# Optimization experiments

Measured on AMD Instinct MI355X. Metric: run time of the kernel, lower is better.

The kernel has to match this reference:

```python
import jax, jax.numpy as jnp
import numpy as np

IN_F = 4096
OUT_F = 4096
RANK = 16
N_BITS = 4
ALPHA = 1.0
GROUP = 128
Q_N = -(2 ** (N_BITS - 1))       # -8 for 4-bit signed
Q_P = 2 ** (N_BITS - 1) - 1      # +7
EPS = 1e-9


def setup_inputs() -> dict:
    key = jax.random.key(0)
    k0, k1, k2, k3, k4, k5 = jax.random.split(key, 6)
    x = jax.random.normal(k0, (8, 1024, IN_F), dtype=jnp.float32)
    w0 = jax.random.normal(k1, (OUT_F, IN_F), dtype=jnp.float32) * 0.02
    lora_a = jax.random.normal(k2, (RANK, IN_F), dtype=jnp.float32) * 0.02
    lora_b = jax.random.normal(k3, (OUT_F, RANK), dtype=jnp.float32) * 0.02
    num_groups = (OUT_F * IN_F) // GROUP
    q_scale = jnp.abs(jax.random.normal(k4, (num_groups,), dtype=jnp.float32)) * 0.01 + 0.005
    bias = jax.random.normal(k5, (OUT_F,), dtype=jnp.float32) * 0.01
    return {"x": x, "w0": w0, "lora_a": lora_a, "lora_b": lora_b,
            "q_scale": q_scale, "bias": bias}


def _quantize_weight(w0, lora_a, lora_b, q_scale):
    # LoRA merge: w_comb = w0 + alpha * (B @ A)   -> (OUT_F, IN_F)
    w_comb = w0 + ALPHA * (lora_b @ lora_a)
    num_groups = w_comb.size // GROUP
    w_g = w_comb.reshape(num_groups, GROUP)          # grouped view
    s = q_scale[:, None]                             # (G, 1) per-group scale
    w_scaled = w_g / (s + EPS)
    clamped = jnp.clip(w_scaled, Q_N, Q_P)
    q_int = jnp.round(clamped)
    w_q = (q_int * s).reshape(w_comb.shape)          # dequantized fake-quant weight
    return w_q


def reference(x, w0, lora_a, lora_b, q_scale, bias):
    w_q = _quantize_weight(w0, lora_a, lora_b, q_scale)
    # F.linear(x, w_q) + bias : (B, S, IN) @ (IN, OUT)
    return jnp.einsum('bsi,oi->bso', x, w_q) + bias
```

## Files before the change

### kernel.cpp

```cpp
#include <hip/hip_runtime.h>
#include <hip/hip_bf16.h>
#include <stdint.h>
#include <stddef.h>

#define IN_F   4096
#define OUT_F  4096
#define RANK   16
#define GROUP  128
#define M_TOT  8192

#define BM     256
#define BN     256
#define BK     32
#define NIT    (IN_F / BK)
#define HALF_B 16384
#define TILE_B 32768
#define LDS_B  (3 * TILE_B)

typedef __bf16 bf16_t;
typedef __bf16 bf16x4 __attribute__((ext_vector_type(4)));
typedef __bf16 bf16x8 __attribute__((ext_vector_type(8)));
typedef float  f32x4  __attribute__((ext_vector_type(4)));

__device__ static inline void load_lds16(const void* g, void* l) {
  __builtin_amdgcn_global_load_lds(
      (const __attribute__((address_space(1))) unsigned int*)g,
      (__attribute__((address_space(3))) unsigned int*)l,
      16, 0, 0);
}

__global__ void __launch_bounds__(256)
quant_kernel(const float* __restrict__ w0, const float* __restrict__ la,
             const float* __restrict__ lb, const float* __restrict__ qs,
             bf16_t* __restrict__ wq)
{
  const int o = blockIdx.y;
  const int i = blockIdx.x * 1024 + threadIdx.x * 4;

  __shared__ float lbr[RANK];
  if (threadIdx.x < RANK) lbr[threadIdx.x] = lb[o * RANK + threadIdx.x];
  __syncthreads();

  const size_t off = (size_t)o * IN_F + i;
  const float4 w = *(const float4*)(w0 + off);
  float a0 = w.x, a1 = w.y, a2 = w.z, a3 = w.w;
  #pragma unroll
  for (int r = 0; r < RANK; ++r) {
    const float4 av = *(const float4*)(la + (size_t)r * IN_F + i);
    const float bv = lbr[r];
    a0 = fmaf(bv, av.x, a0);
    a1 = fmaf(bv, av.y, a1);
    a2 = fmaf(bv, av.z, a2);
    a3 = fmaf(bv, av.w, a3);
  }
  const float s   = qs[o * (IN_F / GROUP) + (i >> 7)];
  const float inv = 1.0f / (s + 1e-9f);
  const float q0 = rintf(fminf(fmaxf(a0 * inv, -8.0f), 7.0f)) * s;
  const float q1 = rintf(fminf(fmaxf(a1 * inv, -8.0f), 7.0f)) * s;
  const float q2 = rintf(fminf(fmaxf(a2 * inv, -8.0f), 7.0f)) * s;
  const float q3 = rintf(fminf(fmaxf(a3 * inv, -8.0f), 7.0f)) * s;
  bf16x4 v;
  v[0] = (bf16_t)q0; v[1] = (bf16_t)q1; v[2] = (bf16_t)q2; v[3] = (bf16_t)q3;
  *(bf16x4*)(wq + off) = v;
}

__global__ void __launch_bounds__(256)
castx_kernel(const float* __restrict__ x, bf16_t* __restrict__ xb)
{
  const size_t i = ((size_t)blockIdx.x * 256 + threadIdx.x) * 8;
  const float4 a = *(const float4*)(x + i);
  const float4 b = *(const float4*)(x + i + 4);
  bf16x8 v;
  v[0] = (bf16_t)a.x; v[1] = (bf16_t)a.y; v[2] = (bf16_t)a.z; v[3] = (bf16_t)a.w;
  v[4] = (bf16_t)b.x; v[5] = (bf16_t)b.y; v[6] = (bf16_t)b.z; v[7] = (bf16_t)b.w;
  *(bf16x8*)(xb + i) = v;
}

__global__ void __launch_bounds__(512, 2)
gemm_kernel(const bf16_t* __restrict__ A, const bf16_t* __restrict__ Bw,
            const float* __restrict__ bias, float* __restrict__ C)
{
  extern __shared__ __align__(16) char smem[];

  const int tid  = threadIdx.x;
  const int lane = tid & 63;
  const int lr   = lane & 15;
  const int quad = lane >> 4;
  const int wid  = tid >> 6;
  const int wm   = wid >> 2;
  const int wn   = wid & 3;

  const int bid = blockIdx.x;
  const int swz = (bid & 7) * 64 + (bid >> 3);
  const int m0  = (swz >> 4) * BM;
  const int n0  = (swz & 15) * BN;

  const int srow = tid >> 2;
  const int scol = ((tid & 3) ^ ((tid >> 3) & 3)) * 8;
  const bf16_t* gA0 = A  + (size_t)(m0 + srow) * IN_F + scol;
  const bf16_t* gA1 = gA0 + (size_t)128 * IN_F;
  const bf16_t* gB0 = Bw + (size_t)(n0 + srow) * IN_F + scol;
  const bf16_t* gB1 = gB0 + (size_t)128 * IN_F;

  const int rswz = (quad ^ ((lr >> 1) & 3)) * 16;
  const int aOff = (wm * 128 + lr) * 64 + rswz;
  const int bOff = (wn * 64  + lr) * 64 + rswz;

  f32x4 acc[8][4];
  #pragma unroll
  for (int i = 0; i < 8; ++i)
    #pragma unroll
    for (int j = 0; j < 4; ++j)
      acc[i][j] = (f32x4){0.f, 0.f, 0.f, 0.f};

  {
    char* b0 = smem;
    char* b1 = smem + TILE_B;
    load_lds16(gA0,      b0 + tid * 16);
    load_lds16(gA1,      b0 + tid * 16 + 8192);
    load_lds16(gB0,      b0 + HALF_B + tid * 16);
    load_lds16(gB1,      b0 + HALF_B + tid * 16 + 8192);
    load_lds16(gA0 + BK, b1 + tid * 16);
    load_lds16(gA1 + BK, b1 + tid * 16 + 8192);
    load_lds16(gB0 + BK, b1 + HALF_B + tid * 16);
    load_lds16(gB1 + BK, b1 + HALF_B + tid * 16 + 8192);
    asm volatile("s_waitcnt vmcnt(4)" ::: "memory");
    __builtin_amdgcn_s_barrier();
  }

  int rb = 0, wb = 2;
  for (int t = 0; t < NIT; ++t) {
    const char* rA   = smem + rb * TILE_B;
    const char* rB   = rA + HALF_B;
    char*       wbuf = smem + wb * TILE_B;

    bf16x8 bfr[4];
    #pragma unroll
    for (int fn = 0; fn < 4; ++fn)
      bfr[fn] = *(const bf16x8*)(rB + bOff + fn * 1024);
    bf16x8 af[4];
    #pragma unroll
    for (int f = 0; f < 4; ++f)
      af[f] = *(const bf16x8*)(rA + aOff + f * 1024);

    if (t + 2 < NIT) {
      const size_t ko = (size_t)(t + 2) * BK;
      load_lds16(gA0 + ko, wbuf + tid * 16);
      load_lds16(gA1 + ko, wbuf + tid * 16 + 8192);
    }

    __builtin_amdgcn_s_barrier();
    asm volatile("s_waitcnt lgkmcnt(0)" ::: "memory");
    __builtin_amdgcn_sched_barrier(0);
    __builtin_amdgcn_s_setprio(1);
    #pragma unroll
    for (int fm = 0; fm < 4; ++fm)
      #pragma unroll
      for (int fn = 0; fn < 4; ++fn)
        acc[fm][fn] = __builtin_amdgcn_mfma_f32_16x16x32_bf16(
            af[fm], bfr[fn], acc[fm][fn], 0, 0, 0);
    __builtin_amdgcn_s_setprio(0);
    __builtin_amdgcn_s_barrier();

    #pragma unroll
    for (int f = 0; f < 4; ++f)
      af[f] = *(const bf16x8*)(rA + aOff + 4096 + f * 1024);

    if (t + 2 < NIT) {
      const size_t ko = (size_t)(t + 2) * BK;
      load_lds16(gB0 + ko, wbuf + HALF_B + tid * 16);
      load_lds16(gB1 + ko, wbuf + HALF_B + tid * 16 + 8192);
    }

    if (t + 2 < NIT) asm volatile("s_waitcnt vmcnt(4)" ::: "memory");
    else             asm volatile("s_waitcnt vmcnt(0)" ::: "memory");
    __builtin_amdgcn_s_barrier();
    asm volatile("s_waitcnt lgkmcnt(0)" ::: "memory");
    __builtin_amdgcn_sched_barrier(0);
    __builtin_amdgcn_s_setprio(1);
    #pragma unroll
    for (int fm = 0; fm < 4; ++fm)
      #pragma unroll
      for (int fn = 0; fn < 4; ++fn)
        acc[4 + fm][fn] = __builtin_amdgcn_mfma_f32_16x16x32_bf16(
            af[fm], bfr[fn], acc[4 + fm][fn], 0, 0, 0);
    __builtin_amdgcn_s_setprio(0);
    __builtin_amdgcn_s_barrier();

    rb = rb + 1; if (rb == 3) rb = 0;
    wb = wb + 1; if (wb == 3) wb = 0;
  }

  #pragma unroll
  for (int fn = 0; fn < 4; ++fn) {
    const int gn = n0 + wn * 64 + fn * 16 + lr;
    const float bv = bias[gn];
    #pragma unroll
    for (int fm = 0; fm < 8; ++fm) {
      const int gm = m0 + wm * 128 + fm * 16 + quad * 4;
      #pragma unroll
      for (int r = 0; r < 4; ++r)
        C[(size_t)(gm + r) * OUT_F + gn] = acc[fm][fn][r] + bv;
    }
  }
}

extern "C" void kernel_launch(void* const* d_in, const int* in_sizes, int n_in,
                              void* d_out, int out_size, void* d_ws, size_t ws_size,
                              hipStream_t stream) {
  const float* x    = (const float*)d_in[0];
  const float* w0   = (const float*)d_in[1];
  const float* la   = (const float*)d_in[2];
  const float* lb   = (const float*)d_in[3];
  const float* qs   = (const float*)d_in[4];
  const float* bias = (const float*)d_in[5];
  float* out = (float*)d_out;

  bf16_t* wq = (bf16_t*)d_ws;
  bf16_t* xb = (bf16_t*)((char*)d_ws + (size_t)OUT_F * IN_F * 2);

  static bool attr_done = false;
  if (!attr_done) {
    (void)hipFuncSetAttribute((const void*)gemm_kernel,
                              hipFuncAttributeMaxDynamicSharedMemorySize,
                              LDS_B);
    attr_done = true;
  }

  quant_kernel<<<dim3(IN_F / 1024, OUT_F), 256, 0, stream>>>(w0, la, lb, qs, wq);
  castx_kernel<<<(M_TOT * IN_F) / (256 * 8), 256, 0, stream>>>(x, xb);
  gemm_kernel<<<dim3((M_TOT / BM) * (OUT_F / BN)), 512, LDS_B, stream>>>(
      xb, wq, bias, out);
}
```

Measured before the change: 549.6 us.

## Software-pipeline LDS fragment reads ahead of MFMA with register double buffering

Restructures the GEMM main loop so the LDS reads for the next half-tile and next K-step (A and B fragments) are issued before the current MFMA block. Ping-pong register buffers for B fragments and an unroll by two make this possible. The explicit lgkmcnt(0) waits and one barrier per phase are removed so LDS latency overlaps with matrix math. The cost is higher register pressure, and the ordering of barriers and vmcnt waits becomes more delicate, which risks hazards.

After: 544.2 us. About the same (-1.0%).

```diff
diff --git a/kernel.cpp b/kernel.cpp
--- a/kernel.cpp
+++ b/kernel.cpp
@@ -113,82 +113,91 @@
     for (int j = 0; j < 4; ++j)
       acc[i][j] = (f32x4){0.f, 0.f, 0.f, 0.f};
 
+  bf16x8 bfr0[4], bfr1[4], afA[4], afB[4];
+
+  auto stageA = [&](int T, char* buf) {
+    const size_t ko = (size_t)T * BK;
+    load_lds16(gA0 + ko, buf + tid * 16);
+    load_lds16(gA1 + ko, buf + tid * 16 + 8192);
+  };
+  auto stageB = [&](int T, char* buf) {
+    const size_t ko = (size_t)T * BK;
+    load_lds16(gB0 + ko, buf + HALF_B + tid * 16);
+    load_lds16(gB1 + ko, buf + HALF_B + tid * 16 + 8192);
+  };
+
+  auto ph_even = [&](int T, const char* rbuf, char* wbuf, bf16x8 (&bcur)[4]) {
+    __builtin_amdgcn_s_barrier();
+    __builtin_amdgcn_sched_barrier(0);
+    if (T + 2 < NIT) stageA(T + 2, wbuf);
+    #pragma unroll
+    for (int f = 0; f < 4; ++f)
+      afB[f] = *(const bf16x8*)(rbuf + aOff + 4096 + f * 1024);
+    __builtin_amdgcn_sched_barrier(0);
+    __builtin_amdgcn_s_setprio(1);
+    #pragma unroll
+    for (int fm = 0; fm < 4; ++fm)
+      #pragma unroll
+      for (int fn = 0; fn < 4; ++fn)
+        acc[fm][fn] = __builtin_amdgcn_mfma_f32_16x16x32_bf16(
+            afA[fm], bcur[fn], acc[fm][fn], 0, 0, 0);
+    __builtin_amdgcn_s_setprio(0);
+  };
+
+  auto ph_odd = [&](int T, const char* rnext, char* wbuf,
+                    bf16x8 (&bcur)[4], bf16x8 (&bnxt)[4]) {
+    if (T + 2 < NIT) asm volatile("s_waitcnt vmcnt(2)" ::: "memory");
+    else             asm volatile("s_waitcnt vmcnt(0)" ::: "memory");
+    __builtin_amdgcn_s_barrier();
+    __builtin_amdgcn_sched_barrier(0);
+    if (T + 2 < NIT) stageB(T + 2, wbuf);
+    if (T + 1 < NIT) {
+      #pragma unroll
+      for (int f = 0; f < 4; ++f)
+        bnxt[f] = *(const bf16x8*)(rnext + HALF_B + bOff + f * 1024);
+      #pragma unroll
+      for (int f = 0; f < 4; ++f)
+        afA[f] = *(const bf16x8*)(rnext + aOff + f * 1024);
+    }
+    __builtin_amdgcn_sched_barrier(0);
+    __builtin_amdgcn_s_setprio(1);
+    #pragma unroll
+    for (int fm = 0; fm < 4; ++fm)
+      #pragma unroll
+      for (int fn = 0; fn < 4; ++fn)
+        acc[4 + fm][fn] = __builtin_amdgcn_mfma_f32_16x16x32_bf16(
+            afB[fm], bcur[fn], acc[4 + fm][fn], 0, 0, 0);
+    __builtin_amdgcn_s_setprio(0);
+  };
+
   {
-    char* b0 = smem;
-    char* b1 = smem + TILE_B;
-    load_lds16(gA0,      b0 + tid * 16);
-    load_lds16(gA1,      b0 + tid * 16 + 8192);
-    load_lds16(gB0,      b0 + HALF_B + tid * 16);
-    load_lds16(gB1,      b0 + HALF_B + tid * 16 + 8192);
-    load_lds16(gA0 + BK, b1 + tid * 16);
-    load_lds16(gA1 + BK, b1 + tid * 16 + 8192);
-    load_lds16(gB0 + BK, b1 + HALF_B + tid * 16);
-    load_lds16(gB1 + BK, b1 + HALF_B + tid * 16 + 8192);
+    stageA(0, smem);          stageB(0, smem);
+    stageA(1, smem + TILE_B); stageB(1, smem + TILE_B);
     asm volatile("s_waitcnt vmcnt(4)" ::: "memory");
     __builtin_amdgcn_s_barrier();
-  }
-
-  int rb = 0, wb = 2;
-  for (int t = 0; t < NIT; ++t) {
-    const char* rA   = smem + rb * TILE_B;
-    const char* rB   = rA + HALF_B;
-    char*       wbuf = smem + wb * TILE_B;
-
-    bf16x8 bfr[4];
-    #pragma unroll
-    for (int fn = 0; fn < 4; ++fn)
-      bfr[fn] = *(const bf16x8*)(rB + bOff + fn * 1024);
-    bf16x8 af[4];
+    __builtin_amdgcn_sched_barrier(0);
     #pragma unroll
     for (int f = 0; f < 4; ++f)
-      af[f] = *(const bf16x8*)(rA + aOff + f * 1024);
-
-    if (t + 2 < NIT) {
-      const size_t ko = (size_t)(t + 2) * BK;
-      load_lds16(gA0 + ko, wbuf + tid * 16);
-      load_lds16(gA1 + ko, wbuf + tid * 16 + 8192);
-    }
-
-    __builtin_amdgcn_s_barrier();
-    asm volatile("s_waitcnt lgkmcnt(0)" ::: "memory");
-    __builtin_amdgcn_sched_barrier(0);
-    __builtin_amdgcn_s_setprio(1);
-    #pragma unroll
-    for (int fm = 0; fm < 4; ++fm)
-      #pragma unroll
-      for (int fn = 0; fn < 4; ++fn)
-        acc[fm][fn] = __builtin_amdgcn_mfma_f32_16x16x32_bf16(
-            af[fm], bfr[fn], acc[fm][fn], 0, 0, 0);
-    __builtin_amdgcn_s_setprio(0);
-    __builtin_amdgcn_s_barrier();
-
+      bfr0[f] = *(const bf16x8*)(smem + HALF_B + bOff + f * 1024);
     #pragma unroll
     for (int f = 0; f < 4; ++f)
-      af[f] = *(const bf16x8*)(rA + aOff + 4096 + f * 1024);
-
-    if (t + 2 < NIT) {
-      const size_t ko = (size_t)(t + 2) * BK;
-      load_lds16(gB0 + ko, wbuf + HALF_B + tid * 16);
-      load_lds16(gB1 + ko, wbuf + HALF_B + tid * 16 + 8192);
-    }
-
-    if (t + 2 < NIT) asm volatile("s_waitcnt vmcnt(4)" ::: "memory");
-    else             asm volatile("s_waitcnt vmcnt(0)" ::: "memory");
-    __builtin_amdgcn_s_barrier();
-    asm volatile("s_waitcnt lgkmcnt(0)" ::: "memory");
-    __builtin_amdgcn_sched_barrier(0);
-    __builtin_amdgcn_s_setprio(1);
-    #pragma unroll
-    for (int fm = 0; fm < 4; ++fm)
-      #pragma unroll
-      for (int fn = 0; fn < 4; ++fn)
-        acc[4 + fm][fn] = __builtin_amdgcn_mfma_f32_16x16x32_bf16(
-            af[fm], bfr[fn], acc[4 + fm][fn], 0, 0, 0);
-    __builtin_amdgcn_s_setprio(0);
-    __builtin_amdgcn_s_barrier();
-
-    rb = rb + 1; if (rb == 3) rb = 0;
-    wb = wb + 1; if (wb == 3) wb = 0;
+      afA[f] = *(const bf16x8*)(smem + aOff + f * 1024);
+  }
+
+  int rb = 0;
+  for (int tt = 0; tt < NIT; tt += 2) {
+    const int rb1 = (rb + 1 == 3) ? 0 : rb + 1;
+    const int rb2 = (rb1 + 1 == 3) ? 0 : rb1 + 1;
+    char* b_rb  = smem + rb  * TILE_B;
+    char* b_rb1 = smem + rb1 * TILE_B;
+    char* b_rb2 = smem + rb2 * TILE_B;
+
+    ph_even(tt,     b_rb,  b_rb2, bfr0);
+    ph_odd (tt,     b_rb1, b_rb2, bfr0, bfr1);
+    ph_even(tt + 1, b_rb1, b_rb,  bfr1);
+    ph_odd (tt + 1, b_rb2, b_rb,  bfr1, bfr0);
+
+    rb = rb2;
   }
 
   #pragma unroll
```

## Double K-tile depth to 64 with two-buffer LDS pipeline and four-phase compute

Applied to the files above, without the earlier changes.

Raises the GEMM K-step from 32 to 64 and replaces the triple-buffered 32-deep LDS ring with two 64 KB buffers. Each K-step now runs four MFMA phases, and global-to-LDS staging of A for the next step and B for the step after is spread across those phases. The LDS swizzle changes to an 8-slot XOR scheme that matches the 128-byte rows. The aim is to halve the number of loop iterations and barriers per FLOP and keep more loads in flight. In exchange it uses 128 KB of LDS per block, which may allow only one resident block per CU instead of the two the launch bounds ask for, and the buffer-reuse ordering is more intricate.

Measured after the change: 529.9 us. -3.6%, faster.

```diff
diff --git a/kernel.cpp b/kernel.cpp
--- a/kernel.cpp
+++ b/kernel.cpp
@@ -11,11 +11,10 @@
 
 #define BM     256
 #define BN     256
-#define BK     32
-#define NIT    (IN_F / BK)
-#define HALF_B 16384
-#define TILE_B 32768
-#define LDS_B  (3 * TILE_B)
+#define BK     64
+#define NKS    (IN_F / BK)
+#define BUF_B  65536
+#define LDS_B  (2 * BUF_B)
 
 typedef __bf16 bf16_t;
 typedef __bf16 bf16x4 __attribute__((ext_vector_type(4)));
@@ -95,16 +94,17 @@
   const int m0  = (swz >> 4) * BM;
   const int n0  = (swz & 15) * BN;
 
-  const int srow = tid >> 2;
-  const int scol = ((tid & 3) ^ ((tid >> 3) & 3)) * 8;
-  const bf16_t* gA0 = A  + (size_t)(m0 + srow) * IN_F + scol;
-  const bf16_t* gA1 = gA0 + (size_t)128 * IN_F;
-  const bf16_t* gB0 = Bw + (size_t)(n0 + srow) * IN_F + scol;
-  const bf16_t* gB1 = gB0 + (size_t)128 * IN_F;
-
-  const int rswz = (quad ^ ((lr >> 1) & 3)) * 16;
-  const int aOff = (wm * 128 + lr) * 64 + rswz;
-  const int bOff = (wn * 64  + lr) * 64 + rswz;
+  const int srow = tid >> 3;
+  const int scol = ((tid & 7) ^ (srow & 7)) * 8;
+  const bf16_t* gA = A  + (size_t)(m0 + srow) * IN_F + scol;
+  const bf16_t* gB = Bw + (size_t)(n0 + srow) * IN_F + scol;
+  const bf16_t* gA1 = gA + (size_t)128 * IN_F;
+  const bf16_t* gB1 = gB + (size_t)128 * IN_F;
+
+  const int sslot = (quad ^ (lr & 7)) * 16;
+  const int aBase = wm * 16384 + lr * 128 + sslot;
+  const int bBase = 32768 + (wn >> 1) * 16384 + (wn & 1) * 8192
+                  + lr * 128 + sslot;
 
   f32x4 acc[8][4];
   #pragma unroll
@@ -113,82 +113,69 @@
     for (int j = 0; j < 4; ++j)
       acc[i][j] = (f32x4){0.f, 0.f, 0.f, 0.f};
 
-  {
-    char* b0 = smem;
-    char* b1 = smem + TILE_B;
-    load_lds16(gA0,      b0 + tid * 16);
-    load_lds16(gA1,      b0 + tid * 16 + 8192);
-    load_lds16(gB0,      b0 + HALF_B + tid * 16);
-    load_lds16(gB1,      b0 + HALF_B + tid * 16 + 8192);
-    load_lds16(gA0 + BK, b1 + tid * 16);
-    load_lds16(gA1 + BK, b1 + tid * 16 + 8192);
-    load_lds16(gB0 + BK, b1 + HALF_B + tid * 16);
-    load_lds16(gB1 + BK, b1 + HALF_B + tid * 16 + 8192);
-    asm volatile("s_waitcnt vmcnt(4)" ::: "memory");
-    __builtin_amdgcn_s_barrier();
-  }
-
-  int rb = 0, wb = 2;
-  for (int t = 0; t < NIT; ++t) {
-    const char* rA   = smem + rb * TILE_B;
-    const char* rB   = rA + HALF_B;
-    char*       wbuf = smem + wb * TILE_B;
-
-    bf16x8 bfr[4];
+  bf16x8 bfr[4][2];
+  bf16x8 af[2][2];
+
+  auto stageHalf = [&](const bf16_t* g0, int ks, char* halfdst) {
+    const bf16_t* g = g0 + (size_t)ks * BK;
+    load_lds16(g, halfdst + tid * 16);
+    load_lds16(g + (size_t)64 * IN_F, halfdst + tid * 16 + 8192);
+  };
+
+  stageHalf(gB,  0, smem + 32768);
+  stageHalf(gB1, 0, smem + 49152);
+  stageHalf(gA,  0, smem + 0);
+  stageHalf(gA1, 0, smem + 16384);
+  stageHalf(gB,  1, smem + BUF_B + 32768);
+  stageHalf(gB1, 1, smem + BUF_B + 49152);
+  asm volatile("s_waitcnt vmcnt(4)" ::: "memory");
+  __builtin_amdgcn_s_barrier();
+
+  for (int ks = 0; ks < NKS; ++ks) {
+    char* rbuf = smem + (ks & 1) * BUF_B;
+    char* obuf = smem + ((ks & 1) ^ 1) * BUF_B;
+
     #pragma unroll
-    for (int fn = 0; fn < 4; ++fn)
-      bfr[fn] = *(const bf16x8*)(rB + bOff + fn * 1024);
-    bf16x8 af[4];
-    #pragma unroll
-    for (int f = 0; f < 4; ++f)
-      af[f] = *(const bf16x8*)(rA + aOff + f * 1024);
-
-    if (t + 2 < NIT) {
-      const size_t ko = (size_t)(t + 2) * BK;
-      load_lds16(gA0 + ko, wbuf + tid * 16);
-      load_lds16(gA1 + ko, wbuf + tid * 16 + 8192);
+    for (int p = 0; p < 4; ++p) {
+      if (p == 0) {
+        #pragma unroll
+        for (int fn = 0; fn < 4; ++fn)
+          #pragma unroll
+          for (int kk = 0; kk < 2; ++kk)
+            bfr[fn][kk] = *(const bf16x8*)(rbuf + ((bBase + fn * 2048) ^ (kk << 6)));
+      }
+      #pragma unroll
+      for (int i = 0; i < 2; ++i)
+        #pragma unroll
+        for (int kk = 0; kk < 2; ++kk)
+          af[i][kk] = *(const bf16x8*)(rbuf + ((aBase + p * 4096 + i * 2048) ^ (kk << 6)));
+
+      if (p == 0 && ks + 1 < NKS) stageHalf(gA,  ks + 1, obuf + 0);
+      if (p == 1) {
+        if (ks + 1 < NKS) stageHalf(gA1, ks + 1, obuf + 16384);
+        if (ks + 2 < NKS) stageHalf(gB,  ks + 2, rbuf + 32768);
+      }
+      if (p == 2 && ks + 2 < NKS) stageHalf(gB1, ks + 2, rbuf + 49152);
+
+      __builtin_amdgcn_s_barrier();
+      asm volatile("s_waitcnt lgkmcnt(0)" ::: "memory");
+      __builtin_amdgcn_sched_barrier(0);
+      __builtin_amdgcn_s_setprio(1);
+      #pragma unroll
+      for (int kk = 0; kk < 2; ++kk)
+        #pragma unroll
+        for (int i = 0; i < 2; ++i)
+          #pragma unroll
+          for (int fn = 0; fn < 4; ++fn)
+            acc[2 * p + i][fn] = __builtin_amdgcn_mfma_f32_16x16x32_bf16(
+                af[i][kk], bfr[fn][kk], acc[2 * p + i][fn], 0, 0, 0);
+      __builtin_amdgcn_s_setprio(0);
+      if (p == 3) {
+        if (ks + 2 < NKS)      asm volatile("s_waitcnt vmcnt(4)" ::: "memory");
+        else if (ks + 1 < NKS) asm volatile("s_waitcnt vmcnt(0)" ::: "memory");
+      }
+      __builtin_amdgcn_s_barrier();
     }
-
-    __builtin_amdgcn_s_barrier();
-    asm volatile("s_waitcnt lgkmcnt(0)" ::: "memory");
-    __builtin_amdgcn_sched_barrier(0);
-    __builtin_amdgcn_s_setprio(1);
-    #pragma unroll
-    for (int fm = 0; fm < 4; ++fm)
-      #pragma unroll
-      for (int fn = 0; fn < 4; ++fn)
-        acc[fm][fn] = __builtin_amdgcn_mfma_f32_16x16x32_bf16(
-            af[fm], bfr[fn], acc[fm][fn], 0, 0, 0);
-    __builtin_amdgcn_s_setprio(0);
-    __builtin_amdgcn_s_barrier();
-
-    #pragma unroll
-    for (int f = 0; f < 4; ++f)
-      af[f] = *(const bf16x8*)(rA + aOff + 4096 + f * 1024);
-
-    if (t + 2 < NIT) {
-      const size_t ko = (size_t)(t + 2) * BK;
-      load_lds16(gB0 + ko, wbuf + HALF_B + tid * 16);
-      load_lds16(gB1 + ko, wbuf + HALF_B + tid * 16 + 8192);
-    }
-
-    if (t + 2 < NIT) asm volatile("s_waitcnt vmcnt(4)" ::: "memory");
-    else             asm volatile("s_waitcnt vmcnt(0)" ::: "memory");
-    __builtin_amdgcn_s_barrier();
-    asm volatile("s_waitcnt lgkmcnt(0)" ::: "memory");
-    __builtin_amdgcn_sched_barrier(0);
-    __builtin_amdgcn_s_setprio(1);
-    #pragma unroll
-    for (int fm = 0; fm < 4; ++fm)
-      #pragma unroll
-      for (int fn = 0; fn < 4; ++fn)
-        acc[4 + fm][fn] = __builtin_amdgcn_mfma_f32_16x16x32_bf16(
-            af[fm], bfr[fn], acc[4 + fm][fn], 0, 0, 0);
-    __builtin_amdgcn_s_setprio(0);
-    __builtin_amdgcn_s_barrier();
-
-    rb = rb + 1; if (rb == 3) rb = 0;
-    wb = wb + 1; if (wb == 3) wb = 0;
   }
 
   #pragma unroll
```
